# Optimization experiments

Hardware: AMD Instinct MI355X
Metric: run time of the kernel (lower is better)

The kernel has to match this reference:

```python
import jax, jax.numpy as jnp
import numpy as np

H = 1024   # hidden_size
NH = 16    # num_heads
HD = H // NH
B, S = 2, 2048


def setup_inputs() -> dict:
    key = jax.random.key(0)
    ks = jax.random.split(key, 6)
    std = 0.02
    x = jax.random.normal(ks[0], (B, S, H), dtype=jnp.float32)
    w_qkv = jax.random.normal(ks[1], (3 * H, H), dtype=jnp.float32) * std
    b_qkv = jnp.zeros((3 * H,), dtype=jnp.float32)
    ln_g = jnp.ones((H,), dtype=jnp.float32)
    ln_b = jnp.zeros((H,), dtype=jnp.float32)
    w_ent = jax.random.normal(ks[2], (1, H), dtype=jnp.float32) * std
    b_ent = jnp.zeros((1,), dtype=jnp.float32)
    w_out = jax.random.normal(ks[3], (H, H), dtype=jnp.float32) * std
    b_out = jnp.zeros((H,), dtype=jnp.float32)
    return {"x": x, "ln_g": ln_g, "ln_b": ln_b, "w_qkv": w_qkv, "b_qkv": b_qkv,
            "w_ent": w_ent, "b_ent": b_ent, "w_out": w_out, "b_out": b_out}


def reference(x, ln_g, ln_b, w_qkv, b_qkv, w_ent, b_ent, w_out, b_out):
    b, s, h = x.shape
    scale = 1.0 / jnp.sqrt(jnp.float32(HD))
    TEMP = 0.1  # fixed softmax temperature

    # LayerNorm (eps=1e-6)
    mu = jnp.mean(x, axis=-1, keepdims=True)
    var = jnp.mean(jnp.square(x - mu), axis=-1, keepdims=True)
    xn = (x - mu) / jnp.sqrt(var + 1e-6) * ln_g + ln_b

    # QKV projection -> [B, S, 3, NH, HD] -> q,k,v each [B, NH, S, HD]
    qkv = xn @ w_qkv.T + b_qkv
    qkv = qkv.reshape(b, s, 3, NH, HD).transpose(2, 0, 3, 1, 4)
    q, k, v = qkv[0], qkv[1], qkv[2]

    # Scaled causal scores [B, NH, S, S]
    scores = jnp.einsum('bhqd,bhkd->bhqk', q, k) * scale
    causal = jnp.tril(jnp.ones((s, s), dtype=bool))
    scores = jnp.where(causal[None, None], scores, -jnp.inf)

    # Sharpened softmax (temperature 0.1); dropout is identity in eval
    probs = jax.nn.softmax(scores / TEMP, axis=-1)

    # Entropy gate over keys: sigmoid proj on post-LN x, clamped [0.1, 2.0]
    gate = jax.nn.sigmoid(xn @ w_ent.T + b_ent)        # [B, S, 1]
    gate = jnp.clip(gate, 0.1, 2.0)[:, None, None, :, 0]  # [B, 1, 1, S]
    probs = probs * gate

    # Weighted values -> merge heads -> output projection, scaled by 0.1
    out = jnp.einsum('bhqk,bhkd->bhqd', probs, v)
    out = out.transpose(0, 2, 1, 3).reshape(b, s, h)
    return (out @ w_out.T + b_out) * 0.1
```

## Files before the change

kernel.cpp:

```cpp
#include <hip/hip_runtime.h>

typedef __bf16 bf16x8 __attribute__((ext_vector_type(8)));
typedef float floatx4 __attribute__((ext_vector_type(4)));
typedef unsigned short u16;

#define LOG2E 1.44269504088896340736f
#define BF16_ONE 0x3F80u

static __device__ __forceinline__ float bf2f(u16 u) {
  union { unsigned int i; float f; } c; c.i = ((unsigned int)u) << 16; return c.f;
}
static __device__ __forceinline__ u16 f2bf(float f) {
  union { float f; unsigned int i; } c; c.f = f;
  unsigned int x = c.i;
  unsigned int r = (x >> 16) & 1u;
  x += 0x7fffu + r;
  return (u16)(x >> 16);
}
static __device__ __forceinline__ u16 f2bf_rne(float f) {
  __bf16 h = (__bf16)f;
  union { __bf16 h; u16 u; } c; c.h = h; return c.u;
}
static __device__ __forceinline__ float fast_exp2(float x) {
#if __has_builtin(__builtin_amdgcn_exp2f)
  return __builtin_amdgcn_exp2f(x);
#else
  return exp2f(x);
#endif
}
static __device__ __forceinline__ float ldp(const void* p, int i, bool isbf) {
  return isbf ? bf2f(((const u16*)p)[i]) : ((const float*)p)[i];
}

__global__ __launch_bounds__(256) void conv2_kernel(
    const void* __restrict__ src0, u16* __restrict__ dst0, int n8_0,
    const void* __restrict__ src1, u16* __restrict__ dst1, int n8_1,
    const u16* __restrict__ probe)
{
  bool isbf = (probe[0] == BF16_ONE);
  int i = blockIdx.x * 256 + threadIdx.x;
  const void* src = src0; u16* dst = dst0;
  if (i >= n8_0) { i -= n8_0; src = src1; dst = dst1; if (i >= n8_1) return; }
  if (isbf) {
    ((uint4*)dst)[i] = ((const uint4*)src)[i];
  } else {
    const float4* s = (const float4*)src;
    float4 a = s[2 * i], b = s[2 * i + 1];
    u16 o[8] = {f2bf(a.x), f2bf(a.y), f2bf(a.z), f2bf(a.w),
                f2bf(b.x), f2bf(b.y), f2bf(b.z), f2bf(b.w)};
    *(uint4*)(&dst[8 * i]) = *(uint4*)o;
  }
}

static __device__ __forceinline__ float blockSum(float v, float* red, int wave, int lane) {
  #pragma unroll
  for (int o = 32; o > 0; o >>= 1) v += __shfl_xor(v, o);
  __syncthreads();
  if (lane == 0) red[wave] = v;
  __syncthreads();
  return red[0] + red[1] + red[2] + red[3];
}

__global__ __launch_bounds__(256) void ln_gate_kernel(
    const void* __restrict__ x, const void* __restrict__ g, const void* __restrict__ bta,
    const void* __restrict__ w_ent, const void* __restrict__ b_ent,
    u16* __restrict__ xn, float* __restrict__ gate, const u16* __restrict__ probe)
{
  __shared__ float red[4];
  bool isbf = (probe[0] == BF16_ONE);
  int row = blockIdx.x;
  int tid = threadIdx.x;
  int wave = tid >> 6, lane = tid & 63;

  float v[4];
  #pragma unroll
  for (int i = 0; i < 4; ++i) {
    size_t idx = (size_t)row * 1024 + tid + 256 * i;
    v[i] = isbf ? bf2f(((const u16*)x)[idx]) : ((const float*)x)[idx];
  }

  float mu = blockSum(v[0] + v[1] + v[2] + v[3], red, wave, lane) * (1.0f / 1024.0f);

  float vs = 0.f;
  #pragma unroll
  for (int i = 0; i < 4; ++i) { float d = v[i] - mu; vs += d * d; }
  float var = blockSum(vs, red, wave, lane) * (1.0f / 1024.0f);
  float rstd = rsqrtf(var + 1e-6f);

  float gp = 0.f;
  #pragma unroll
  for (int i = 0; i < 4; ++i) {
    int col = tid + 256 * i;
    float xv = (v[i] - mu) * rstd * ldp(g, col, isbf) + ldp(bta, col, isbf);
    xn[(size_t)row * 1024 + col] = f2bf(xv);
    gp += xv * ldp(w_ent, col, isbf);
  }
  float tot = blockSum(gp, red, wave, lane);
  if (tid == 0) {
    float z = tot + ldp(b_ent, 0, isbf);
    float sg = 1.0f / (1.0f + exp2f(-z * LOG2E));
    gate[row] = fminf(fmaxf(sg, 0.1f), 2.0f);
  }
}

#define GEMM_STAGE(Abase, Wbase) \
  { \
    int lrow = lane >> 3; \
    int scb = ((lane & 7) ^ lrow) * 8; \
    _Pragma("unroll") \
    for (int it = 0; it < 4; ++it) { \
      int chunk = wave * 4 + it; \
      int row = chunk * 8 + lrow; \
      __builtin_amdgcn_global_load_lds( \
        (const __attribute__((address_space(1))) void*)&Abase[(size_t)(m0 + row) * K + k0 + scb], \
        (__attribute__((address_space(3))) void*)&As[chunk * 512], 16, 0, 0); \
      __builtin_amdgcn_global_load_lds( \
        (const __attribute__((address_space(1))) void*)&Wbase[(size_t)(n0 + row) * K + k0 + scb], \
        (__attribute__((address_space(3))) void*)&Ws[chunk * 512], 16, 0, 0); \
    } \
  }

#define GEMM_COMPUTE() \
  _Pragma("unroll") \
  for (int kk = 0; kk < 64; kk += 32) { \
    int kkb = kk >> 3; \
    bf16x8 af[4], bfr[4]; \
    _Pragma("unroll") \
    for (int i = 0; i < 4; ++i) \
      af[i] = *(const bf16x8*)(&As[(wm + 16 * i + lr) * 64 + ((kkb + lg) ^ (lr & 7)) * 8]); \
    _Pragma("unroll") \
    for (int j = 0; j < 4; ++j) \
      bfr[j] = *(const bf16x8*)(&Ws[(wn + 16 * j + lr) * 64 + ((kkb + lg) ^ (lr & 7)) * 8]); \
    _Pragma("unroll") \
    for (int i = 0; i < 4; ++i) \
      _Pragma("unroll") \
      for (int j = 0; j < 4; ++j) \
        acc[i][j] = __builtin_amdgcn_mfma_f32_16x16x32_bf16(af[i], bfr[j], acc[i][j], 0, 0, 0); \
  }

__global__ __launch_bounds__(256) void gemm_bt_kernel(
    const u16* __restrict__ A, const u16* __restrict__ W, const void* __restrict__ bias,
    const float* __restrict__ gate, u16* __restrict__ C, int M, int N, int K,
    const u16* __restrict__ probe)
{
  __shared__ __align__(16) u16 As[128 * 64];
  __shared__ __align__(16) u16 Ws[128 * 64];
  int m0 = blockIdx.y * 128, n0 = blockIdx.x * 128;
  int tid = threadIdx.x, wave = tid >> 6, lane = tid & 63;
  int lr = lane & 15, lg = lane >> 4;
  int wm = (wave >> 1) * 64, wn = (wave & 1) * 64;

  floatx4 acc[4][4];
  #pragma unroll
  for (int i = 0; i < 4; ++i)
    #pragma unroll
    for (int j = 0; j < 4; ++j)
      #pragma unroll
      for (int r = 0; r < 4; ++r) acc[i][j][r] = 0.f;

  for (int k0 = 0; k0 < K; k0 += 64) {
    GEMM_STAGE(A, W)
    __syncthreads();
    GEMM_COMPUTE()
    __syncthreads();
  }

  bool isbf = (probe[0] == BF16_ONE);
  bool doGate = (n0 >= 2048);
  float gm[4][4];
  #pragma unroll
  for (int i = 0; i < 4; ++i)
    #pragma unroll
    for (int r = 0; r < 4; ++r)
      gm[i][r] = doGate ? gate[m0 + wm + 16 * i + lg * 4 + r] : 1.0f;

  #pragma unroll
  for (int j = 0; j < 4; ++j) {
    int n = n0 + wn + 16 * j + lr;
    float bv = ldp(bias, n, isbf);
    #pragma unroll
    for (int i = 0; i < 4; ++i) {
      int mbase = m0 + wm + 16 * i + lg * 4;
      #pragma unroll
      for (int r = 0; r < 4; ++r)
        C[(size_t)(mbase + r) * N + n] = f2bf((acc[i][j][r] + bv) * gm[i][r]);
    }
  }
}

__global__ __launch_bounds__(256) void gemm_out_kernel(
    const u16* __restrict__ A, const u16* __restrict__ W, const void* __restrict__ bias,
    void* __restrict__ C, int M, int N, int K, float scale, const u16* __restrict__ probe)
{
  __shared__ __align__(16) u16 As[128 * 64];
  __shared__ __align__(16) u16 Ws[128 * 64];
  int m0 = blockIdx.y * 128, n0 = blockIdx.x * 128;
  int tid = threadIdx.x, wave = tid >> 6, lane = tid & 63;
  int lr = lane & 15, lg = lane >> 4;
  int wm = (wave >> 1) * 64, wn = (wave & 1) * 64;

  floatx4 acc[4][4];
  #pragma unroll
  for (int i = 0; i < 4; ++i)
    #pragma unroll
    for (int j = 0; j < 4; ++j)
      #pragma unroll
      for (int r = 0; r < 4; ++r) acc[i][j][r] = 0.f;

  for (int k0 = 0; k0 < K; k0 += 64) {
    GEMM_STAGE(A, W)
    __syncthreads();
    GEMM_COMPUTE()
    __syncthreads();
  }

  bool isbf = (probe[0] == BF16_ONE);
  #pragma unroll
  for (int j = 0; j < 4; ++j) {
    int n = n0 + wn + 16 * j + lr;
    float bv = ldp(bias, n, isbf);
    #pragma unroll
    for (int i = 0; i < 4; ++i) {
      int mbase = m0 + wm + 16 * i + lg * 4;
      #pragma unroll
      for (int r = 0; r < 4; ++r) {
        float v = (acc[i][j][r] + bv) * scale;
        size_t idx = (size_t)(mbase + r) * N + n;
        if (isbf) ((u16*)C)[idx] = f2bf(v);
        else      ((float*)C)[idx] = v;
      }
    }
  }
}

#define PSTR 72
#define CEXP (1.25f * LOG2E)

template<bool DOA>
static __device__ __forceinline__ void tile_compute(
    const u16* __restrict__ Ks, const u16* __restrict__ Vt,
    u16* __restrict__ psB, u16* __restrict__ psA,
    const bf16x8* qfB, const bf16x8* qfA,
    floatx4* accOB, floatx4* accOA, float& lB, float& lA,
    bool diagB, bool diagA, int wave, int lr, int lg)
{
  int qg = wave * 16 + lr;
  #pragma unroll
  for (int jt = 0; jt < 4; ++jt) {
    floatx4 aB = {0.f, 0.f, 0.f, 0.f};
    floatx4 aA = {0.f, 0.f, 0.f, 0.f};
    __builtin_amdgcn_s_setprio(1);
    #pragma unroll
    for (int kk = 0; kk < 2; ++kk) {
      bf16x8 bk = *(const bf16x8*)(&Ks[(jt * 16 + lr) * 72 + kk * 32 + lg * 8]);
      aB = __builtin_amdgcn_mfma_f32_16x16x32_bf16(bk, qfB[kk], aB, 0, 0, 0);
      if (DOA) aA = __builtin_amdgcn_mfma_f32_16x16x32_bf16(bk, qfA[kk], aA, 0, 0, 0);
    }
    __builtin_amdgcn_s_setprio(0);
    int kbase = jt * 16 + lg * 4;
    u16 pb[4], pa[4];
    #pragma unroll
    for (int r = 0; r < 4; ++r) {
      float eB = fast_exp2(aB[r] * CEXP);
      if (diagB && (kbase + r) > qg) eB = 0.f;
      lB += eB;
      pb[r] = f2bf_rne(eB);
      if (DOA) {
        float eA = fast_exp2(aA[r] * CEXP);
        if (diagA && (kbase + r) > qg) eA = 0.f;
        lA += eA;
        pa[r] = f2bf_rne(eA);
      }
    }
    *(uint2*)(&psB[lr * PSTR + kbase]) = *(uint2*)pb;
    if (DOA) *(uint2*)(&psA[lr * PSTR + kbase]) = *(uint2*)pa;
  }
  bf16x8 apB[2], apA[2];
  #pragma unroll
  for (int kk = 0; kk < 2; ++kk) {
    apB[kk] = *(const bf16x8*)(&psB[lr * PSTR + kk * 32 + lg * 8]);
    if (DOA) apA[kk] = *(const bf16x8*)(&psA[lr * PSTR + kk * 32 + lg * 8]);
  }
  __builtin_amdgcn_s_setprio(1);
  #pragma unroll
  for (int jt = 0; jt < 4; ++jt)
    #pragma unroll
    for (int kk = 0; kk < 2; ++kk) {
      bf16x8 bv = *(const bf16x8*)(&Vt[(jt * 16 + lr) * 72 + kk * 32 + lg * 8]);
      accOB[jt] = __builtin_amdgcn_mfma_f32_16x16x32_bf16(apB[kk], bv, accOB[jt], 0, 0, 0);
      if (DOA) accOA[jt] = __builtin_amdgcn_mfma_f32_16x16x32_bf16(apA[kk], bv, accOA[jt], 0, 0, 0);
    }
  __builtin_amdgcn_s_setprio(0);
}

__global__ __launch_bounds__(256) void attn_kernel(
    const u16* __restrict__ qkv, u16* __restrict__ out)
{
  __shared__ __align__(16) u16 Ks[64 * 72];
  __shared__ __align__(16) u16 Vt[64 * 72];
  __shared__ __align__(16) u16 Ps[2 * 4 * 16 * PSTR];

  int bid = blockIdx.x;
  int xcd = bid & 7, kb = bid >> 3;
  int bh = xcd * 4 + (kb >> 4);
  int pr = kb & 15;
  int h = bh & 15, b = bh >> 4;
  int tid = threadIdx.x, wave = tid >> 6, lane = tid & 63;
  int lr = lane & 15, lg = lane >> 4;
  const int RS = 3072;

  int tA = pr, tB = 31 - pr;

  bf16x8 qfA[2], qfB[2];
  int qrbA = b * 2048 + tA * 64 + wave * 16;
  int qrbB = b * 2048 + tB * 64 + wave * 16;
  #pragma unroll
  for (int kk = 0; kk < 2; ++kk) {
    qfA[kk] = *(const bf16x8*)(&qkv[(size_t)(qrbA + lr) * RS + h * 64 + kk * 32 + lg * 8]);
    qfB[kk] = *(const bf16x8*)(&qkv[(size_t)(qrbB + lr) * RS + h * 64 + kk * 32 + lg * 8]);
  }

  floatx4 accOA[4], accOB[4];
  float lA = 0.f, lB = 0.f;
  #pragma unroll
  for (int jt = 0; jt < 4; ++jt)
    #pragma unroll
    for (int r = 0; r < 4; ++r) { accOA[jt][r] = 0.f; accOB[jt][r] = 0.f; }

  u16* psB = &Ps[(size_t)wave * 16 * PSTR];
  u16* psA = &Ps[(size_t)(4 + wave) * 16 * PSTR];

  int srow = tid >> 3, sc8 = (tid & 7) * 8;
  int vkey = tid & 63, vd0 = (tid >> 6) * 16;

  uint4 kp0, kp1, vp0, vp1;

  {
    int krow0 = b * 2048;
    kp0 = *(const uint4*)(&qkv[(size_t)(krow0 + srow) * RS + 1024 + h * 64 + sc8]);
    kp1 = *(const uint4*)(&qkv[(size_t)(krow0 + 32 + srow) * RS + 1024 + h * 64 + sc8]);
    const u16* vrow = &qkv[(size_t)(krow0 + vkey) * RS + 2048 + h * 64 + vd0];
    vp0 = *(const uint4*)(vrow);
    vp1 = *(const uint4*)(vrow + 8);
  }

  for (int kt = 0; kt <= tB; ++kt) {
    __syncthreads();
    *(uint4*)(&Ks[srow * 72 + sc8]) = kp0;
    *(uint4*)(&Ks[(srow + 32) * 72 + sc8]) = kp1;
    {
      unsigned int ww[8] = {vp0.x, vp0.y, vp0.z, vp0.w, vp1.x, vp1.y, vp1.z, vp1.w};
      #pragma unroll
      for (int i = 0; i < 8; ++i) {
        Vt[(vd0 + 2 * i) * 72 + vkey]     = (u16)(ww[i] & 0xffffu);
        Vt[(vd0 + 2 * i + 1) * 72 + vkey] = (u16)(ww[i] >> 16);
      }
    }
    __syncthreads();

    if (kt < tB) {
      int krow0 = b * 2048 + (kt + 1) * 64;
      kp0 = *(const uint4*)(&qkv[(size_t)(krow0 + srow) * RS + 1024 + h * 64 + sc8]);
      kp1 = *(const uint4*)(&qkv[(size_t)(krow0 + 32 + srow) * RS + 1024 + h * 64 + sc8]);
      const u16* vrow = &qkv[(size_t)(krow0 + vkey) * RS + 2048 + h * 64 + vd0];
      vp0 = *(const uint4*)(vrow);
      vp1 = *(const uint4*)(vrow + 8);
    }

    bool diagB = (kt == tB), diagA = (kt == tA);
    if (kt <= tA)
      tile_compute<true>(Ks, Vt, psB, psA, qfB, qfA, accOB, accOA, lB, lA,
                         diagB, diagA, wave, lr, lg);
    else
      tile_compute<false>(Ks, Vt, psB, psA, qfB, qfA, accOB, accOA, lB, lA,
                          diagB, diagA, wave, lr, lg);
  }

  lB += __shfl_xor(lB, 16); lB += __shfl_xor(lB, 32);
  lA += __shfl_xor(lA, 16); lA += __shfl_xor(lA, 32);
  float liB[4], liA[4];
  #pragma unroll
  for (int r = 0; r < 4; ++r) {
    liB[r] = 1.0f / fmaxf(__shfl(lB, lg * 4 + r), 1e-30f);
    liA[r] = 1.0f / fmaxf(__shfl(lA, lg * 4 + r), 1e-30f);
  }
  #pragma unroll
  for (int jt = 0; jt < 4; ++jt)
    #pragma unroll
    for (int r = 0; r < 4; ++r) {
      int mB = qrbB + lg * 4 + r;
      out[(size_t)mB * 1024 + h * 64 + jt * 16 + lr] = f2bf(accOB[jt][r] * liB[r]);
      int mA = qrbA + lg * 4 + r;
      out[(size_t)mA * 1024 + h * 64 + jt * 16 + lr] = f2bf(accOA[jt][r] * liA[r]);
    }
}

extern "C" void kernel_launch(void* const* d_in, const int* in_sizes, int n_in,
                              void* d_out, int out_size, void* d_ws, size_t ws_size,
                              hipStream_t stream) {
  const void* x     = d_in[0];
  const void* ln_g  = d_in[1];
  const void* ln_b  = d_in[2];
  const void* w_qkv = d_in[3];
  const void* b_qkv = d_in[4];
  const void* w_ent = d_in[5];
  const void* b_ent = d_in[6];
  const void* w_out = d_in[7];
  const void* b_out = d_in[8];
  const u16* probe = (const u16*)ln_g;

  char* ws = (char*)d_ws;
  float* gate    = (float*)(ws);
  u16* xc        = (u16*)(ws + (64u << 10));
  u16* qkvb      = (u16*)(ws + (64u << 10) + (8u << 20));
  u16* w_qkv_c   = (u16*)(ws + (64u << 10) + (32u << 20));
  u16* w_out_c   = (u16*)(ws + (64u << 10) + (38u << 20));

  conv2_kernel<<<2048, 256, 0, stream>>>(w_qkv, w_qkv_c, 393216,
                                         w_out, w_out_c, 131072, probe);

  ln_gate_kernel<<<4096, 256, 0, stream>>>(x, ln_g, ln_b, w_ent, b_ent, xc, gate, probe);
  gemm_bt_kernel<<<dim3(24, 32), 256, 0, stream>>>(xc, w_qkv_c, b_qkv, gate, qkvb, 4096, 3072, 1024, probe);
  attn_kernel<<<512, 256, 0, stream>>>(qkvb, xc );
  gemm_out_kernel<<<dim3(8, 32), 256, 0, stream>>>(xc, w_out_c, b_out, d_out, 4096, 1024, 1024, 0.1f, probe);
}
```

Before: 212.5 us.

## Fuse prep kernels, double-buffer attention K/V, retile output GEMM to 64-row blocks

```diff
diff --git a/kernel.cpp b/kernel.cpp
--- a/kernel.cpp
+++ b/kernel.cpp
@@ -32,26 +32,6 @@
   return isbf ? bf2f(((const u16*)p)[i]) : ((const float*)p)[i];
 }
 
-__global__ __launch_bounds__(256) void conv2_kernel(
-    const void* __restrict__ src0, u16* __restrict__ dst0, int n8_0,
-    const void* __restrict__ src1, u16* __restrict__ dst1, int n8_1,
-    const u16* __restrict__ probe)
-{
-  bool isbf = (probe[0] == BF16_ONE);
-  int i = blockIdx.x * 256 + threadIdx.x;
-  const void* src = src0; u16* dst = dst0;
-  if (i >= n8_0) { i -= n8_0; src = src1; dst = dst1; if (i >= n8_1) return; }
-  if (isbf) {
-    ((uint4*)dst)[i] = ((const uint4*)src)[i];
-  } else {
-    const float4* s = (const float4*)src;
-    float4 a = s[2 * i], b = s[2 * i + 1];
-    u16 o[8] = {f2bf(a.x), f2bf(a.y), f2bf(a.z), f2bf(a.w),
-                f2bf(b.x), f2bf(b.y), f2bf(b.z), f2bf(b.w)};
-    *(uint4*)(&dst[8 * i]) = *(uint4*)o;
-  }
-}
-
 static __device__ __forceinline__ float blockSum(float v, float* red, int wave, int lane) {
   #pragma unroll
   for (int o = 32; o > 0; o >>= 1) v += __shfl_xor(v, o);
@@ -61,15 +41,35 @@
   return red[0] + red[1] + red[2] + red[3];
 }
 
-__global__ __launch_bounds__(256) void ln_gate_kernel(
+__global__ __launch_bounds__(256) void prep_kernel(
+    const void* __restrict__ w_qkv, u16* __restrict__ w_qkv_c,
+    const void* __restrict__ w_out, u16* __restrict__ w_out_c,
     const void* __restrict__ x, const void* __restrict__ g, const void* __restrict__ bta,
     const void* __restrict__ w_ent, const void* __restrict__ b_ent,
     u16* __restrict__ xn, float* __restrict__ gate, const u16* __restrict__ probe)
 {
   __shared__ float red[4];
   bool isbf = (probe[0] == BF16_ONE);
-  int row = blockIdx.x;
+  int blk = blockIdx.x;
   int tid = threadIdx.x;
+
+  if (blk < 2048) {
+    int i = blk * 256 + tid;
+    const void* src = w_qkv; u16* dst = w_qkv_c;
+    if (i >= 393216) { i -= 393216; src = w_out; dst = w_out_c; }
+    if (isbf) {
+      ((uint4*)dst)[i] = ((const uint4*)src)[i];
+    } else {
+      const float4* s = (const float4*)src;
+      float4 a = s[2 * i], b = s[2 * i + 1];
+      u16 o[8] = {f2bf(a.x), f2bf(a.y), f2bf(a.z), f2bf(a.w),
+                  f2bf(b.x), f2bf(b.y), f2bf(b.z), f2bf(b.w)};
+      *(uint4*)(&dst[8 * i]) = *(uint4*)o;
+    }
+    return;
+  }
+
+  int row = blk - 2048;
   int wave = tid >> 6, lane = tid & 63;
 
   float v[4];
@@ -192,36 +192,69 @@
     const u16* __restrict__ A, const u16* __restrict__ W, const void* __restrict__ bias,
     void* __restrict__ C, int M, int N, int K, float scale, const u16* __restrict__ probe)
 {
-  __shared__ __align__(16) u16 As[128 * 64];
+  __shared__ __align__(16) u16 As[64 * 64];
   __shared__ __align__(16) u16 Ws[128 * 64];
-  int m0 = blockIdx.y * 128, n0 = blockIdx.x * 128;
+  int m0 = blockIdx.y * 64, n0 = blockIdx.x * 128;
   int tid = threadIdx.x, wave = tid >> 6, lane = tid & 63;
   int lr = lane & 15, lg = lane >> 4;
-  int wm = (wave >> 1) * 64, wn = (wave & 1) * 64;
-
-  floatx4 acc[4][4];
+  int wn = wave * 32;
+
+  floatx4 acc[4][2];
   #pragma unroll
   for (int i = 0; i < 4; ++i)
     #pragma unroll
-    for (int j = 0; j < 4; ++j)
+    for (int j = 0; j < 2; ++j)
       #pragma unroll
       for (int r = 0; r < 4; ++r) acc[i][j][r] = 0.f;
 
   for (int k0 = 0; k0 < K; k0 += 64) {
-    GEMM_STAGE(A, W)
+    {
+      int lrow = lane >> 3;
+      int scb = ((lane & 7) ^ lrow) * 8;
+      #pragma unroll
+      for (int c = wave; c < 24; c += 4) {
+        if (c < 8) {
+          int row = c * 8 + lrow;
+          __builtin_amdgcn_global_load_lds(
+            (const __attribute__((address_space(1))) void*)&A[(size_t)(m0 + row) * K + k0 + scb],
+            (__attribute__((address_space(3))) void*)&As[c * 512], 16, 0, 0);
+        } else {
+          int cc = c - 8;
+          int row = cc * 8 + lrow;
+          __builtin_amdgcn_global_load_lds(
+            (const __attribute__((address_space(1))) void*)&W[(size_t)(n0 + row) * K + k0 + scb],
+            (__attribute__((address_space(3))) void*)&Ws[cc * 512], 16, 0, 0);
+        }
+      }
+    }
     __syncthreads();
-    GEMM_COMPUTE()
+    #pragma unroll
+    for (int kk = 0; kk < 64; kk += 32) {
+      int kkb = kk >> 3;
+      bf16x8 af[4], bfr[2];
+      #pragma unroll
+      for (int i = 0; i < 4; ++i)
+        af[i] = *(const bf16x8*)(&As[(16 * i + lr) * 64 + ((kkb + lg) ^ (lr & 7)) * 8]);
+      #pragma unroll
+      for (int j = 0; j < 2; ++j)
+        bfr[j] = *(const bf16x8*)(&Ws[(wn + 16 * j + lr) * 64 + ((kkb + lg) ^ (lr & 7)) * 8]);
+      #pragma unroll
+      for (int i = 0; i < 4; ++i)
+        #pragma unroll
+        for (int j = 0; j < 2; ++j)
+          acc[i][j] = __builtin_amdgcn_mfma_f32_16x16x32_bf16(af[i], bfr[j], acc[i][j], 0, 0, 0);
+    }
     __syncthreads();
   }
 
   bool isbf = (probe[0] == BF16_ONE);
   #pragma unroll
-  for (int j = 0; j < 4; ++j) {
+  for (int j = 0; j < 2; ++j) {
     int n = n0 + wn + 16 * j + lr;
     float bv = ldp(bias, n, isbf);
     #pragma unroll
     for (int i = 0; i < 4; ++i) {
-      int mbase = m0 + wm + 16 * i + lg * 4;
+      int mbase = m0 + 16 * i + lg * 4;
       #pragma unroll
       for (int r = 0; r < 4; ++r) {
         float v = (acc[i][j][r] + bv) * scale;
@@ -236,59 +269,43 @@
 #define PSTR 72
 #define CEXP (1.25f * LOG2E)
 
-template<bool DOA>
-static __device__ __forceinline__ void tile_compute(
-    const u16* __restrict__ Ks, const u16* __restrict__ Vt,
-    u16* __restrict__ psB, u16* __restrict__ psA,
-    const bf16x8* qfB, const bf16x8* qfA,
-    floatx4* accOB, floatx4* accOA, float& lB, float& lA,
-    bool diagB, bool diagA, int wave, int lr, int lg)
+static __device__ __forceinline__ void attn_half(
+    const u16* __restrict__ Ks, const u16* __restrict__ Vt, u16* __restrict__ ps,
+    const bf16x8* qf, floatx4* accO, float& l,
+    bool diag, int qg, int lr, int lg)
 {
-  int qg = wave * 16 + lr;
   #pragma unroll
   for (int jt = 0; jt < 4; ++jt) {
-    floatx4 aB = {0.f, 0.f, 0.f, 0.f};
-    floatx4 aA = {0.f, 0.f, 0.f, 0.f};
+    floatx4 a = {0.f, 0.f, 0.f, 0.f};
     __builtin_amdgcn_s_setprio(1);
     #pragma unroll
     for (int kk = 0; kk < 2; ++kk) {
       bf16x8 bk = *(const bf16x8*)(&Ks[(jt * 16 + lr) * 72 + kk * 32 + lg * 8]);
-      aB = __builtin_amdgcn_mfma_f32_16x16x32_bf16(bk, qfB[kk], aB, 0, 0, 0);
-      if (DOA) aA = __builtin_amdgcn_mfma_f32_16x16x32_bf16(bk, qfA[kk], aA, 0, 0, 0);
+      a = __builtin_amdgcn_mfma_f32_16x16x32_bf16(bk, qf[kk], a, 0, 0, 0);
     }
     __builtin_amdgcn_s_setprio(0);
     int kbase = jt * 16 + lg * 4;
-    u16 pb[4], pa[4];
+    u16 pb[4];
     #pragma unroll
     for (int r = 0; r < 4; ++r) {
-      float eB = fast_exp2(aB[r] * CEXP);
-      if (diagB && (kbase + r) > qg) eB = 0.f;
-      lB += eB;
-      pb[r] = f2bf_rne(eB);
-      if (DOA) {
-        float eA = fast_exp2(aA[r] * CEXP);
-        if (diagA && (kbase + r) > qg) eA = 0.f;
-        lA += eA;
-        pa[r] = f2bf_rne(eA);
-      }
-    }
-    *(uint2*)(&psB[lr * PSTR + kbase]) = *(uint2*)pb;
-    if (DOA) *(uint2*)(&psA[lr * PSTR + kbase]) = *(uint2*)pa;
-  }
-  bf16x8 apB[2], apA[2];
-  #pragma unroll
-  for (int kk = 0; kk < 2; ++kk) {
-    apB[kk] = *(const bf16x8*)(&psB[lr * PSTR + kk * 32 + lg * 8]);
-    if (DOA) apA[kk] = *(const bf16x8*)(&psA[lr * PSTR + kk * 32 + lg * 8]);
-  }
+      float e = fast_exp2(a[r] * CEXP);
+      if (diag && (kbase + r) > qg) e = 0.f;
+      l += e;
+      pb[r] = f2bf_rne(e);
+    }
+    *(uint2*)(&ps[lr * PSTR + kbase]) = *(uint2*)pb;
+  }
+  bf16x8 ap[2];
+  #pragma unroll
+  for (int kk = 0; kk < 2; ++kk)
+    ap[kk] = *(const bf16x8*)(&ps[lr * PSTR + kk * 32 + lg * 8]);
   __builtin_amdgcn_s_setprio(1);
   #pragma unroll
   for (int jt = 0; jt < 4; ++jt)
     #pragma unroll
     for (int kk = 0; kk < 2; ++kk) {
       bf16x8 bv = *(const bf16x8*)(&Vt[(jt * 16 + lr) * 72 + kk * 32 + lg * 8]);
-      accOB[jt] = __builtin_amdgcn_mfma_f32_16x16x32_bf16(apB[kk], bv, accOB[jt], 0, 0, 0);
-      if (DOA) accOA[jt] = __builtin_amdgcn_mfma_f32_16x16x32_bf16(apA[kk], bv, accOA[jt], 0, 0, 0);
+      accO[jt] = __builtin_amdgcn_mfma_f32_16x16x32_bf16(ap[kk], bv, accO[jt], 0, 0, 0);
     }
   __builtin_amdgcn_s_setprio(0);
 }
@@ -296,9 +313,9 @@
 __global__ __launch_bounds__(256) void attn_kernel(
     const u16* __restrict__ qkv, u16* __restrict__ out)
 {
-  __shared__ __align__(16) u16 Ks[64 * 72];
-  __shared__ __align__(16) u16 Vt[64 * 72];
-  __shared__ __align__(16) u16 Ps[2 * 4 * 16 * PSTR];
+  __shared__ __align__(16) u16 Ks[2][64 * 72];
+  __shared__ __align__(16) u16 Vt[2][64 * 72];
+  __shared__ __align__(16) u16 Ps[4][16 * PSTR];
 
   int bid = blockIdx.x;
   int xcd = bid & 7, kb = bid >> 3;
@@ -327,53 +344,54 @@
     #pragma unroll
     for (int r = 0; r < 4; ++r) { accOA[jt][r] = 0.f; accOB[jt][r] = 0.f; }
 
-  u16* psB = &Ps[(size_t)wave * 16 * PSTR];
-  u16* psA = &Ps[(size_t)(4 + wave) * 16 * PSTR];
+  u16* ps = Ps[wave];
 
   int srow = tid >> 3, sc8 = (tid & 7) * 8;
   int vkey = tid & 63, vd0 = (tid >> 6) * 16;
 
   uint4 kp0, kp1, vp0, vp1;
 
-  {
-    int krow0 = b * 2048;
+  auto LOADK = [&](int kt) {
+    int krow0 = b * 2048 + kt * 64;
     kp0 = *(const uint4*)(&qkv[(size_t)(krow0 + srow) * RS + 1024 + h * 64 + sc8]);
     kp1 = *(const uint4*)(&qkv[(size_t)(krow0 + 32 + srow) * RS + 1024 + h * 64 + sc8]);
     const u16* vrow = &qkv[(size_t)(krow0 + vkey) * RS + 2048 + h * 64 + vd0];
     vp0 = *(const uint4*)(vrow);
     vp1 = *(const uint4*)(vrow + 8);
-  }
-
+  };
+  auto COMMIT = [&](int bi) {
+    u16* ksb = (u16*)Ks[bi];
+    u16* vtb = (u16*)Vt[bi];
+    *(uint4*)(&ksb[srow * 72 + sc8]) = kp0;
+    *(uint4*)(&ksb[(srow + 32) * 72 + sc8]) = kp1;
+    unsigned int ww[8] = {vp0.x, vp0.y, vp0.z, vp0.w, vp1.x, vp1.y, vp1.z, vp1.w};
+    #pragma unroll
+    for (int i = 0; i < 8; ++i) {
+      vtb[(vd0 + 2 * i) * 72 + vkey]     = (u16)(ww[i] & 0xffffu);
+      vtb[(vd0 + 2 * i + 1) * 72 + vkey] = (u16)(ww[i] >> 16);
+    }
+  };
+
+  LOADK(0);
+  COMMIT(0);
+  LOADK(1);
+  __syncthreads();
+
+  int qg = wave * 16 + lr;
   for (int kt = 0; kt <= tB; ++kt) {
-    __syncthreads();
-    *(uint4*)(&Ks[srow * 72 + sc8]) = kp0;
-    *(uint4*)(&Ks[(srow + 32) * 72 + sc8]) = kp1;
-    {
-      unsigned int ww[8] = {vp0.x, vp0.y, vp0.z, vp0.w, vp1.x, vp1.y, vp1.z, vp1.w};
-      #pragma unroll
-      for (int i = 0; i < 8; ++i) {
-        Vt[(vd0 + 2 * i) * 72 + vkey]     = (u16)(ww[i] & 0xffffu);
-        Vt[(vd0 + 2 * i + 1) * 72 + vkey] = (u16)(ww[i] >> 16);
-      }
-    }
-    __syncthreads();
-
+    int cur = kt & 1;
+    bool diagB = (kt == tB), diagA = (kt == tA);
+    if (kt <= tA) {
+      attn_half(Ks[cur], Vt[cur], ps, qfB, accOB, lB, diagB, qg, lr, lg);
+      attn_half(Ks[cur], Vt[cur], ps, qfA, accOA, lA, diagA, qg, lr, lg);
+    } else {
+      attn_half(Ks[cur], Vt[cur], ps, qfB, accOB, lB, diagB, qg, lr, lg);
+    }
     if (kt < tB) {
-      int krow0 = b * 2048 + (kt + 1) * 64;
-      kp0 = *(const uint4*)(&qkv[(size_t)(krow0 + srow) * RS + 1024 + h * 64 + sc8]);
-      kp1 = *(const uint4*)(&qkv[(size_t)(krow0 + 32 + srow) * RS + 1024 + h * 64 + sc8]);
-      const u16* vrow = &qkv[(size_t)(krow0 + vkey) * RS + 2048 + h * 64 + vd0];
-      vp0 = *(const uint4*)(vrow);
-      vp1 = *(const uint4*)(vrow + 8);
-    }
-
-    bool diagB = (kt == tB), diagA = (kt == tA);
-    if (kt <= tA)
-      tile_compute<true>(Ks, Vt, psB, psA, qfB, qfA, accOB, accOA, lB, lA,
-                         diagB, diagA, wave, lr, lg);
-    else
-      tile_compute<false>(Ks, Vt, psB, psA, qfB, qfA, accOB, accOA, lB, lA,
-                          diagB, diagA, wave, lr, lg);
+      COMMIT(cur ^ 1);
+      if (kt + 2 <= tB) LOADK(kt + 2);
+      __syncthreads();
+    }
   }
 
   lB += __shfl_xor(lB, 16); lB += __shfl_xor(lB, 32);
@@ -416,11 +434,9 @@
   u16* w_qkv_c   = (u16*)(ws + (64u << 10) + (32u << 20));
   u16* w_out_c   = (u16*)(ws + (64u << 10) + (38u << 20));
 
-  conv2_kernel<<<2048, 256, 0, stream>>>(w_qkv, w_qkv_c, 393216,
-                                         w_out, w_out_c, 131072, probe);
-
-  ln_gate_kernel<<<4096, 256, 0, stream>>>(x, ln_g, ln_b, w_ent, b_ent, xc, gate, probe);
+  prep_kernel<<<6144, 256, 0, stream>>>(w_qkv, w_qkv_c, w_out, w_out_c,
+                                        x, ln_g, ln_b, w_ent, b_ent, xc, gate, probe);
   gemm_bt_kernel<<<dim3(24, 32), 256, 0, stream>>>(xc, w_qkv_c, b_qkv, gate, qkvb, 4096, 3072, 1024, probe);
   attn_kernel<<<512, 256, 0, stream>>>(qkvb, xc );
-  gemm_out_kernel<<<dim3(8, 32), 256, 0, stream>>>(xc, w_out_c, b_out, d_out, 4096, 1024, 1024, 0.1f, probe);
-}
+  gemm_out_kernel<<<dim3(8, 64), 256, 0, stream>>>(xc, w_out_c, b_out, d_out, 4096, 1024, 1024, 0.1f, probe);
+}
```

Measured after the change: 207.9 us. 2.2% less time.
